# Kernel tuning notes

Hardware: AMD Instinct MI355X
Metric: run time of the kernel (lower is better)

## Reference

```python
import jax, jax.numpy as jnp
import numpy as np

EPS = 1e-7  # tf.keras.backend.epsilon()
ROUTING_ITERS = 3


def setup_inputs() -> dict:
    key = jax.random.key(0)
    k1, k2 = jax.random.split(key)
    B, I, Din = 64, 4096, 8
    N, D = 10, 16
    inputs = jax.random.normal(k1, (B, I, Din), dtype=jnp.float32)
    # glorot_uniform-ish init for W [I, N, Din, D]
    limit = (6.0 / (Din + D)) ** 0.5
    W = jax.random.uniform(k2, (I, N, Din, D), dtype=jnp.float32, minval=-limit, maxval=limit)
    return {"inputs": inputs, "W": W}


def _elementwise_squash(s):
    # Original squashes over axis=-2 of [B,1,N,1,D], a size-1 axis ->
    # the reduce_sum is a no-op and squash becomes elementwise.
    sq = s * s
    scale = sq / (1.0 + sq) / jnp.sqrt(sq + EPS)
    return scale * s


def reference(inputs, W):
    # inputs: [B, I, Din], W: [I, N, Din, D]
    # u_hat[b,i,n,d] = sum_p inputs[b,i,p] * W[i,n,p,d]  (the tile+matmul)
    u_hat = jnp.einsum('bip,inpd->bind', inputs, W)  # [B, I, N, D]
    B, I, N, D = u_hat.shape
    b = jnp.zeros((B, I, N, 1), dtype=u_hat.dtype)
    v = None
    for it in range(ROUTING_ITERS):
        c = jax.nn.softmax(b, axis=2)                 # [B, I, N, 1]
        s = jnp.sum(c * u_hat, axis=1)                # [B, N, D]
        v = _elementwise_squash(s)                    # [B, N, D]
        if it < ROUTING_ITERS - 1:
            # agreement: sum over D -> [B, I, N, 1]
            b = b + jnp.sum(u_hat * v[:, None, :, :], axis=-1, keepdims=True)
    # original: squeeze(v[B,1,N,1,D], axis=1) -> [B, N, 1, D]
    return v[:, :, None, :]
```

## Files before the change

kernel.cpp:

```cpp
#include <hip/hip_runtime.h>
#include <math.h>

#define B_ 64
#define I_ 4096
#define P_ 8
#define N_ 10
#define D_ 16
#define ND_ 160
#define BND_ (B_*ND_)
#define EPS_ 1e-7f

#define IPB_ 8
#define NBLK_ (I_ / IPB_)
#define WTILE_ (N_ * P_ * D_)
#define NSTR_ 144
#define ILSTR_ (N_ * NSTR_)
#define RBLK_ 320

#define NGRP_ 16
#define GSZ_  32
#define LINEW_ 16
#define SLOTW_ ((NGRP_ + 1) * LINEW_)
#define NSLOT_ 5

template<int CTRL>
__device__ __forceinline__ float dpp_bcast(float v) {
    int r = __builtin_amdgcn_update_dpp(0, __float_as_int(v), CTRL, 0xF, 0xF, true);
    return __int_as_float(r);
}

__device__ __forceinline__ void agent_store_f2(float* dst, float a, float b) {
    float2 v; v.x = a; v.y = b;
    unsigned long long u; __builtin_memcpy(&u, &v, 8);
    __hip_atomic_store((unsigned long long*)dst, u,
                       __ATOMIC_RELAXED, __HIP_MEMORY_SCOPE_AGENT);
}
__device__ __forceinline__ float2 agent_load_f2(const float* src) {
    unsigned long long u = __hip_atomic_load((unsigned long long*)src,
                       __ATOMIC_RELAXED, __HIP_MEMORY_SCOPE_AGENT);
    float2 v; __builtin_memcpy(&v, &u, 8); return v;
}
__device__ __forceinline__ float agent_load_f(const float* src) {
    return __hip_atomic_load((float*)src, __ATOMIC_RELAXED,
                             __HIP_MEMORY_SCOPE_AGENT);
}
__device__ __forceinline__ void agent_store_f(float* dst, float v) {
    __hip_atomic_store(dst, v, __ATOMIC_RELAXED, __HIP_MEMORY_SCOPE_AGENT);
}

__device__ __forceinline__ void gridbar(unsigned* cnt, int slot) {
    __syncthreads();
    if (threadIdx.x == 0) {
        unsigned* base = cnt + slot * SLOTW_;
        const unsigned g = (unsigned)blockIdx.x & (NGRP_ - 1u);
        unsigned* gl = base + g * LINEW_;
        unsigned* rp = base + NGRP_ * LINEW_;
        __builtin_amdgcn_fence(__ATOMIC_RELEASE, "workgroup");
        unsigned gold = __hip_atomic_fetch_add(&gl[0], 1u,
                            __ATOMIC_RELAXED, __HIP_MEMORY_SCOPE_AGENT);
        unsigned epoch = gold / (unsigned)GSZ_;
        if ((gold % (unsigned)GSZ_) == (unsigned)GSZ_ - 1u)
            __hip_atomic_fetch_add(&rp[0], 1u,
                __ATOMIC_RELAXED, __HIP_MEMORY_SCOPE_AGENT);
        long long t0 = (long long)__builtin_amdgcn_s_memrealtime();
        if ((unsigned)blockIdx.x < (unsigned)NGRP_) {
            unsigned rtgt = (epoch + 1u) * (unsigned)NGRP_;
            while (__hip_atomic_load(&rp[0], __ATOMIC_RELAXED,
                                     __HIP_MEMORY_SCOPE_AGENT) < rtgt) {
                __builtin_amdgcn_s_sleep(8);
                if ((long long)__builtin_amdgcn_s_memrealtime() - t0 > 2000000LL)
                    break;
            }
            __hip_atomic_store(&gl[1], epoch + 1u,
                __ATOMIC_RELAXED, __HIP_MEMORY_SCOPE_AGENT);
        }
        while (__hip_atomic_load(&gl[1], __ATOMIC_RELAXED,
                                 __HIP_MEMORY_SCOPE_AGENT) < epoch + 1u) {
            __builtin_amdgcn_s_sleep(8);
            if ((long long)__builtin_amdgcn_s_memrealtime() - t0 > 2000000LL)
                break;
        }
        __builtin_amdgcn_fence(__ATOMIC_ACQUIRE, "workgroup");
    }
    __syncthreads();
}

__global__ __launch_bounds__(256, 2)
void digitcaps_fused(const float* __restrict__ x, const float* __restrict__ W,
                     float* __restrict__ part, float* __restrict__ Vc,
                     float* __restrict__ out, unsigned* __restrict__ cnt)
{
    __shared__ float wsh[IPB_ * ILSTR_];
    __shared__ float rsm[4][32];
    const int t = threadIdx.x;
    const int lane = t & 63;
    const int ds  = lane & 7;
    const int np  = (lane >> 3) & 1;
    const int bl2 = lane >> 4;
    const int wv  = t >> 6;
    const int bb  = wv * 16 + bl2 * 4;
    const int i0  = blockIdx.x * IPB_;

    {
        const float4* __restrict__ Wg = (const float4*)(W + (size_t)i0 * WTILE_);
        float4* __restrict__ Ws = (float4*)wsh;
#pragma unroll
        for (int c0 = 0; c0 < (IPB_ * WTILE_) / (4 * 256); ++c0) {
            int c  = c0 * 256 + t;
            int il = c / 320;
            int r  = c - il * 320;
            int n  = r >> 5;
            int s  = r & 31;
            Ws[il * 360 + n * 36 + s] = Wg[c];
        }
    }
    __syncthreads();

    float vprev = 0.f;

    for (int it = 0; it < 3; ++it) {
        const bool uni = (it == 0);

        float vc[4][5][2];
        if (!uni) {
#pragma unroll
            for (int j = 0; j < 4; ++j)
#pragma unroll
                for (int k = 0; k < 5; ++k) {
                    float2 v = agent_load_f2(Vc + (size_t)(bb + j) * ND_
                                             + (np + 2 * k) * D_ + 2 * ds);
                    vc[j][k][0] = v.x; vc[j][k][1] = v.y;
                }
        }

        float acc[4][5][2];
#pragma unroll
        for (int j = 0; j < 4; ++j)
#pragma unroll
            for (int k = 0; k < 5; ++k) { acc[j][k][0] = 0.f; acc[j][k][1] = 0.f; }

        float xv[4][P_];
#pragma unroll
        for (int j = 0; j < 4; ++j) {
            const float4* xp = (const float4*)(x + ((size_t)(bb + j) * I_ + i0) * P_);
            float4 a0 = xp[0], a1 = xp[1];
            xv[j][0]=a0.x; xv[j][1]=a0.y; xv[j][2]=a0.z; xv[j][3]=a0.w;
            xv[j][4]=a1.x; xv[j][5]=a1.y; xv[j][6]=a1.z; xv[j][7]=a1.w;
        }

#pragma unroll 1
        for (int il = 0; il < IPB_; ++il) {
            const float* __restrict__ Wb = wsh + il * ILSTR_ + np * NSTR_ + 2 * ds;

            float tv[4][5][2];
#pragma unroll
            for (int k = 0; k < 5; ++k) {
#pragma unroll
                for (int j = 0; j < 4; ++j) { tv[j][k][0] = 0.f; tv[j][k][1] = 0.f; }
#pragma unroll
                for (int p = 0; p < P_; ++p) {
                    float2 w = *(const float2*)(Wb + k * 2 * NSTR_ + p * D_);
#pragma unroll
                    for (int j = 0; j < 4; ++j) {
                        tv[j][k][0] = fmaf(w.x, xv[j][p], tv[j][k][0]);
                        tv[j][k][1] = fmaf(w.y, xv[j][p], tv[j][k][1]);
                    }
                }
            }

            float xn[4][P_];
            if (il + 1 < IPB_) {
#pragma unroll
                for (int j = 0; j < 4; ++j) {
                    const float4* xp = (const float4*)(x + ((size_t)(bb + j) * I_
                                                            + i0 + il + 1) * P_);
                    float4 a0 = xp[0], a1 = xp[1];
                    xn[j][0]=a0.x; xn[j][1]=a0.y; xn[j][2]=a0.z; xn[j][3]=a0.w;
                    xn[j][4]=a1.x; xn[j][5]=a1.y; xn[j][6]=a1.z; xn[j][7]=a1.w;
                }
            }

            if (uni) {
#pragma unroll
                for (int j = 0; j < 4; ++j)
#pragma unroll
                    for (int k = 0; k < 5; ++k) {
                        acc[j][k][0] += tv[j][k][0];
                        acc[j][k][1] += tv[j][k][1];
                    }
            } else {
#pragma unroll
                for (int j = 0; j < 4; ++j) {
                    float e[5];
                    float m = -1e30f;
#pragma unroll
                    for (int k = 0; k < 5; ++k) {
                        float l = fmaf(tv[j][k][1], vc[j][k][1],
                                       tv[j][k][0] * vc[j][k][0]);
                        l += dpp_bcast<0xB1>(l);
                        l += dpp_bcast<0x4E>(l);
                        l += dpp_bcast<0x141>(l);
                        e[k] = l;
                        m = fmaxf(m, l);
                    }
                    m = fmaxf(m, dpp_bcast<0x140>(m));
                    float se = 0.f;
#pragma unroll
                    for (int k = 0; k < 5; ++k) { e[k] = __expf(e[k] - m); se += e[k]; }
                    se += dpp_bcast<0x140>(se);
                    float inv = 1.f / se;
#pragma unroll
                    for (int k = 0; k < 5; ++k) {
                        float cn = e[k] * inv;
                        acc[j][k][0] = fmaf(cn, tv[j][k][0], acc[j][k][0]);
                        acc[j][k][1] = fmaf(cn, tv[j][k][1], acc[j][k][1]);
                    }
                }
            }

            if (il + 1 < IPB_) {
#pragma unroll
                for (int j = 0; j < 4; ++j)
#pragma unroll
                    for (int p = 0; p < P_; ++p) xv[j][p] = xn[j][p];
            }
        }

#pragma unroll
        for (int j = 0; j < 4; ++j) {
            float* __restrict__ dst = part + (size_t)blockIdx.x * BND_
                                      + (size_t)(bb + j) * ND_ + np * D_ + 2 * ds;
#pragma unroll
            for (int k = 0; k < 5; ++k)
                agent_store_f2(dst + k * 2 * D_, acc[j][k][0], acc[j][k][1]);
        }

        gridbar(cnt, it * 2);

        if (blockIdx.x < RBLK_) {
            const int oi = t & 31;
            const int tp = t >> 5;
            const int o  = blockIdx.x * 32 + oi;
            float s = 0.f;
            const float* __restrict__ p0 = part + (size_t)(tp * 64) * BND_ + o;
#pragma unroll 8
            for (int j = 0; j < 64; ++j)
                s += agent_load_f(p0 + (size_t)j * BND_);
            s += __shfl_down(s, 32);
            if ((t & 63) < 32) rsm[t >> 6][oi] = s;
            __syncthreads();
            if (t < 32) {
                float tot = (rsm[0][t] + rsm[1][t]) + (rsm[2][t] + rsm[3][t]);
                tot *= uni ? 0.1f : 1.0f;
                float sq = tot * tot;
                float v = tot * (sq / ((1.f + sq) * sqrtf(sq + EPS_)));
                int o2 = blockIdx.x * 32 + t;
                if (it == 0)      { vprev = v;      agent_store_f(Vc + o2, vprev); }
                else if (it == 1) { vprev += v;     agent_store_f(Vc + o2, vprev); }
                else              out[o2] = v;
            }
        }

        if (it < 2) gridbar(cnt, it * 2 + 1);
    }
}

extern "C" void kernel_launch(void* const* d_in, const int* in_sizes, int n_in,
                              void* d_out, int out_size, void* d_ws, size_t ws_size,
                              hipStream_t stream)
{
    const float* x = (const float*)d_in[0];
    const float* W = (const float*)d_in[1];
    float* out = (float*)d_out;

    float* part = (float*)d_ws;
    float* Vc   = part + (size_t)NBLK_ * BND_;
    unsigned* cnt = (unsigned*)(Vc + BND_);

    hipMemsetAsync(cnt, 0, NSLOT_ * SLOTW_ * sizeof(unsigned), stream);

    digitcaps_fused<<<dim3(NBLK_), dim3(256), 0, stream>>>(x, W, part, Vc, out, cnt);
}
```

Baseline: 176.3 us.

## Spread partial reduction over all blocks, stage x in LDS, tighten grid barrier spin

The cross-block reduction now runs on all 512 blocks instead of 320. Each block handles 20 outputs, with 240 threads doing 8-byte agent loads over row chunks and a final LDS sum. The block's x tile is loaded into shared memory once rather than reloaded from global memory in every routing iteration. The grid barrier spins with a shorter sleep, and the leader blocks no longer wait on the second flag. This adds LDS use and a serial 48-term sum per output, in exchange for spreading the reduction work across more blocks and cutting barrier latency.

```diff
diff --git a/kernel.cpp b/kernel.cpp
--- a/kernel.cpp
+++ b/kernel.cpp
@@ -15,7 +15,7 @@
 #define WTILE_ (N_ * P_ * D_)
 #define NSTR_ 144
 #define ILSTR_ (N_ * NSTR_)
-#define RBLK_ 320
+#define XSTR_ 68
 
 #define NGRP_ 16
 #define GSZ_  32
@@ -39,10 +39,6 @@
     unsigned long long u = __hip_atomic_load((unsigned long long*)src,
                        __ATOMIC_RELAXED, __HIP_MEMORY_SCOPE_AGENT);
     float2 v; __builtin_memcpy(&v, &u, 8); return v;
-}
-__device__ __forceinline__ float agent_load_f(const float* src) {
-    return __hip_atomic_load((float*)src, __ATOMIC_RELAXED,
-                             __HIP_MEMORY_SCOPE_AGENT);
 }
 __device__ __forceinline__ void agent_store_f(float* dst, float v) {
     __hip_atomic_store(dst, v, __ATOMIC_RELAXED, __HIP_MEMORY_SCOPE_AGENT);
@@ -67,18 +63,19 @@
             unsigned rtgt = (epoch + 1u) * (unsigned)NGRP_;
             while (__hip_atomic_load(&rp[0], __ATOMIC_RELAXED,
                                      __HIP_MEMORY_SCOPE_AGENT) < rtgt) {
-                __builtin_amdgcn_s_sleep(8);
+                __builtin_amdgcn_s_sleep(1);
                 if ((long long)__builtin_amdgcn_s_memrealtime() - t0 > 2000000LL)
                     break;
             }
             __hip_atomic_store(&gl[1], epoch + 1u,
                 __ATOMIC_RELAXED, __HIP_MEMORY_SCOPE_AGENT);
-        }
-        while (__hip_atomic_load(&gl[1], __ATOMIC_RELAXED,
-                                 __HIP_MEMORY_SCOPE_AGENT) < epoch + 1u) {
-            __builtin_amdgcn_s_sleep(8);
-            if ((long long)__builtin_amdgcn_s_memrealtime() - t0 > 2000000LL)
-                break;
+        } else {
+            while (__hip_atomic_load(&gl[1], __ATOMIC_RELAXED,
+                                     __HIP_MEMORY_SCOPE_AGENT) < epoch + 1u) {
+                __builtin_amdgcn_s_sleep(1);
+                if ((long long)__builtin_amdgcn_s_memrealtime() - t0 > 2000000LL)
+                    break;
+            }
         }
         __builtin_amdgcn_fence(__ATOMIC_ACQUIRE, "workgroup");
     }
@@ -91,7 +88,8 @@
                      float* __restrict__ out, unsigned* __restrict__ cnt)
 {
     __shared__ float wsh[IPB_ * ILSTR_];
-    __shared__ float rsm[4][32];
+    __shared__ float xsh[B_ * XSTR_];
+    __shared__ float4 rsm4[48][5];
     const int t = threadIdx.x;
     const int lane = t & 63;
     const int ds  = lane & 7;
@@ -114,6 +112,15 @@
             Ws[il * 360 + n * 36 + s] = Wg[c];
         }
     }
+    {
+        const int xb = t >> 2;
+        const int xc = t & 3;
+        const float4* __restrict__ xg = (const float4*)(x + ((size_t)xb * I_ + i0) * P_);
+        float4* __restrict__ xd = (float4*)(xsh + xb * XSTR_);
+#pragma unroll
+        for (int q = 0; q < 4; ++q)
+            xd[xc * 4 + q] = xg[xc * 4 + q];
+    }
     __syncthreads();
 
     float vprev = 0.f;
@@ -139,19 +146,19 @@
 #pragma unroll
             for (int k = 0; k < 5; ++k) { acc[j][k][0] = 0.f; acc[j][k][1] = 0.f; }
 
-        float xv[4][P_];
-#pragma unroll
-        for (int j = 0; j < 4; ++j) {
-            const float4* xp = (const float4*)(x + ((size_t)(bb + j) * I_ + i0) * P_);
-            float4 a0 = xp[0], a1 = xp[1];
-            xv[j][0]=a0.x; xv[j][1]=a0.y; xv[j][2]=a0.z; xv[j][3]=a0.w;
-            xv[j][4]=a1.x; xv[j][5]=a1.y; xv[j][6]=a1.z; xv[j][7]=a1.w;
-        }
-
 #pragma unroll 1
         for (int il = 0; il < IPB_; ++il) {
             const float* __restrict__ Wb = wsh + il * ILSTR_ + np * NSTR_ + 2 * ds;
 
+            float xr[4][P_];
+#pragma unroll
+            for (int j = 0; j < 4; ++j) {
+                const float4* xp = (const float4*)(xsh + (bb + j) * XSTR_ + il * P_);
+                float4 a0 = xp[0], a1 = xp[1];
+                xr[j][0]=a0.x; xr[j][1]=a0.y; xr[j][2]=a0.z; xr[j][3]=a0.w;
+                xr[j][4]=a1.x; xr[j][5]=a1.y; xr[j][6]=a1.z; xr[j][7]=a1.w;
+            }
+
             float tv[4][5][2];
 #pragma unroll
             for (int k = 0; k < 5; ++k) {
@@ -162,21 +169,9 @@
                     float2 w = *(const float2*)(Wb + k * 2 * NSTR_ + p * D_);
 #pragma unroll
                     for (int j = 0; j < 4; ++j) {
-                        tv[j][k][0] = fmaf(w.x, xv[j][p], tv[j][k][0]);
-                        tv[j][k][1] = fmaf(w.y, xv[j][p], tv[j][k][1]);
-                    }
-                }
-            }
-
-            float xn[4][P_];
-            if (il + 1 < IPB_) {
-#pragma unroll
-                for (int j = 0; j < 4; ++j) {
-                    const float4* xp = (const float4*)(x + ((size_t)(bb + j) * I_
-                                                            + i0 + il + 1) * P_);
-                    float4 a0 = xp[0], a1 = xp[1];
-                    xn[j][0]=a0.x; xn[j][1]=a0.y; xn[j][2]=a0.z; xn[j][3]=a0.w;
-                    xn[j][4]=a1.x; xn[j][5]=a1.y; xn[j][6]=a1.z; xn[j][7]=a1.w;
+                        tv[j][k][0] = fmaf(w.x, xr[j][p], tv[j][k][0]);
+                        tv[j][k][1] = fmaf(w.y, xr[j][p], tv[j][k][1]);
+                    }
                 }
             }
 
@@ -217,13 +212,6 @@
                     }
                 }
             }
-
-            if (il + 1 < IPB_) {
-#pragma unroll
-                for (int j = 0; j < 4; ++j)
-#pragma unroll
-                    for (int p = 0; p < P_; ++p) xv[j][p] = xn[j][p];
-            }
         }
 
 #pragma unroll
@@ -237,28 +225,35 @@
 
         gridbar(cnt, it * 2);
 
-        if (blockIdx.x < RBLK_) {
-            const int oi = t & 31;
-            const int tp = t >> 5;
-            const int o  = blockIdx.x * 32 + oi;
-            float s = 0.f;
-            const float* __restrict__ p0 = part + (size_t)(tp * 64) * BND_ + o;
-#pragma unroll 8
-            for (int j = 0; j < 64; ++j)
-                s += agent_load_f(p0 + (size_t)j * BND_);
-            s += __shfl_down(s, 32);
-            if ((t & 63) < 32) rsm[t >> 6][oi] = s;
-            __syncthreads();
-            if (t < 32) {
-                float tot = (rsm[0][t] + rsm[1][t]) + (rsm[2][t] + rsm[3][t]);
-                tot *= uni ? 0.1f : 1.0f;
-                float sq = tot * tot;
-                float v = tot * (sq / ((1.f + sq) * sqrtf(sq + EPS_)));
-                int o2 = blockIdx.x * 32 + t;
-                if (it == 0)      { vprev = v;      agent_store_f(Vc + o2, vprev); }
-                else if (it == 1) { vprev += v;     agent_store_f(Vc + o2, vprev); }
-                else              out[o2] = v;
-            }
+        const int o0 = blockIdx.x * 20;
+        if (t < 240) {
+            const int fg = t % 5;
+            const int tp = t / 5;
+            const int r0 = (tp < 32) ? tp * 11 : 352 + (tp - 32) * 10;
+            const int rc = (tp < 32) ? 11 : 10;
+            float4 s4 = {0.f, 0.f, 0.f, 0.f};
+            const float* __restrict__ p0 = part + (size_t)r0 * BND_ + o0 + fg * 4;
+            for (int r = 0; r < rc; ++r) {
+                float2 a = agent_load_f2(p0 + (size_t)r * BND_);
+                float2 b = agent_load_f2(p0 + (size_t)r * BND_ + 2);
+                s4.x += a.x; s4.y += a.y; s4.z += b.x; s4.w += b.y;
+            }
+            rsm4[tp][fg] = s4;
+        }
+        __syncthreads();
+        if (t < 20) {
+            const int fg = t >> 2, c = t & 3;
+            float tot = 0.f;
+#pragma unroll
+            for (int tp = 0; tp < 48; ++tp)
+                tot += ((const float*)&rsm4[tp][fg])[c];
+            tot *= uni ? 0.1f : 1.0f;
+            float sq = tot * tot;
+            float v = tot * (sq / ((1.f + sq) * sqrtf(sq + EPS_)));
+            const int o2 = o0 + t;
+            if (it == 0)      { vprev = v;   agent_store_f(Vc + o2, vprev); }
+            else if (it == 1) { vprev += v;  agent_store_f(Vc + o2, vprev); }
+            else              out[o2] = v;
         }
 
         if (it < 2) gridbar(cnt, it * 2 + 1);
```

New measurement: 169.9 us. 1.04x faster.
